# Performance work log

Hardware: AMD Instinct MI355X
Metric: run time of the kernel (lower is better)

## Reference

```python
import jax, jax.numpy as jnp
import numpy as np

LATENT, TARGET, EMB_SCALE = 2048, 64, 0.1
STEPS_IGNORE, STEPS_PREDICT = 2, 3


def conv(x, w, b, stride=(1, 1), padding=((0, 0), (0, 0))):
    y = jax.lax.conv_general_dilated(x, w, stride, padding,
                                     dimension_numbers=('NCHW', 'OIHW', 'NCHW'))
    return y + b[None, :, None, None]


def setup_inputs() -> dict:
    key = jax.random.key(0)
    ks = jax.random.split(key, 24)
    B = 64
    inp = {}
    inp['images'] = jax.random.normal(ks[0], (B, 3, 256, 256), jnp.float32)
    inp['rnd'] = jax.random.randint(ks[1], (B * 49,), 0, 16, jnp.int32)
    s = lambda *sh: 1.0 / np.sqrt(np.prod(sh[1:]))
    # stand-in encoder: conv3->256 k8 s8, relu, conv256->2048 1x1, relu, global mean pool
    inp['enc_w1'] = jax.random.normal(ks[2], (256, 3, 8, 8), jnp.float32) * s(256, 3, 8, 8)
    inp['enc_b1'] = jnp.zeros((256,), jnp.float32)
    inp['enc_w2'] = jax.random.normal(ks[3], (LATENT, 256, 1, 1), jnp.float32) * s(LATENT, 256)
    inp['enc_b2'] = jnp.zeros((LATENT,), jnp.float32)
    # PixelCNN: 5 residual blocks, each 4 convs
    inp['pc_w1'] = jax.random.normal(ks[4], (5, 256, LATENT, 1, 1), jnp.float32) * s(0, LATENT)
    inp['pc_b1'] = jnp.zeros((5, 256), jnp.float32)
    inp['pc_w2'] = jax.random.normal(ks[5], (5, 256, 256, 1, 3), jnp.float32) * s(0, 256 * 3)
    inp['pc_b2'] = jnp.zeros((5, 256), jnp.float32)
    inp['pc_w3'] = jax.random.normal(ks[6], (5, 256, 256, 2, 1), jnp.float32) * s(0, 256 * 2)
    inp['pc_b3'] = jnp.zeros((5, 256), jnp.float32)
    inp['pc_w4'] = jax.random.normal(ks[7], (5, LATENT, 256, 1, 1), jnp.float32) * s(0, 256)
    inp['pc_b4'] = jnp.zeros((5, LATENT), jnp.float32)
    inp['z2t_w'] = jax.random.normal(ks[8], (TARGET, LATENT, 1, 1), jnp.float32) * s(0, LATENT)
    inp['z2t_b'] = jnp.zeros((TARGET,), jnp.float32)
    inp['c2p_w'] = jax.random.normal(ks[9], (STEPS_PREDICT, TARGET, LATENT, 1, 1), jnp.float32) * s(0, LATENT)
    inp['c2p_b'] = jnp.zeros((STEPS_PREDICT, TARGET), jnp.float32)
    return inp


def _forward(images, enc_w1, enc_b1, enc_w2, enc_b2,
             pc_w1, pc_b1, pc_w2, pc_b2, pc_w3, pc_b3, pc_w4, pc_b4,
             z2t_w, z2t_b, c2p_w, c2p_b, rnd):
    B = images.shape[0]
    # ---- patch extraction: (B,3,256,256) -> (B*49,3,64,64), r-major then c ----
    patches = jnp.stack([images[:, :, r * 32:r * 32 + 64, c * 32:c * 32 + 64]
                         for r in range(7) for c in range(7)], axis=1)
    patches = patches.reshape(-1, 3, 64, 64)
    N = patches.shape[0]
    # ---- vectorized random border masking (replaces per-patch python loop) ----
    r = (rnd // 4).astype(jnp.int32)           # (N,)
    c = (rnd % 4).astype(jnp.int32)
    idx = jnp.arange(64, dtype=jnp.int32)
    row_ok = (idx[None, :] >= r[:, None]) & (idx[None, :] < r[:, None] + 60)  # (N,64)
    col_ok = (idx[None, :] >= c[:, None]) & (idx[None, :] < c[:, None] + 60)
    mask = row_ok[:, None, :, None] & col_ok[:, None, None, :]                # (N,1,64,64)
    patches = jnp.where(mask, patches, jnp.float32(-1.0))
    # ---- stand-in encoder (resnet_v1 replaced by small conv stack) ----
    h = jax.nn.relu(conv(patches, enc_w1, enc_b1, stride=(8, 8)))  # (N,256,8,8)
    h = jax.nn.relu(conv(h, enc_w2, enc_b2))                        # (N,2048,8,8)
    latents = h.mean(axis=(2, 3))                                   # (N,2048)
    latents = latents.reshape(B, 7, 7, LATENT).transpose(0, 3, 1, 2)  # (B,2048,7,7)
    # ---- PixelCNN context ----
    x = latents
    for k in range(5):
        y = jax.nn.relu(conv(x, pc_w1[k], pc_b1[k]))
        y = jax.nn.relu(conv(y, pc_w2[k], pc_b2[k], padding=((0, 0), (1, 1))))
        y = jax.nn.relu(conv(y, pc_w3[k], pc_b3[k], padding=((1, 0), (0, 0))))
        y = conv(y, pc_w4[k], pc_b4[k])
        x = jax.nn.relu(y + x)
    context = x
    # ---- contrastive loss ----
    targets = conv(latents, z2t_w, z2t_b).transpose(0, 2, 3, 1).reshape(-1, TARGET)  # (B*49,64)
    col_dim, row_dim = 7, 7
    loss = jnp.float32(0.0)
    for i in range(STEPS_IGNORE, STEPS_IGNORE + STEPS_PREDICT):
        col_dim_i = col_dim - i - 1
        total = B * col_dim_i * row_dim
        preds = conv(context, c2p_w[i - STEPS_IGNORE], c2p_b[i - STEPS_IGNORE])
        preds = preds[:, :, :-(i + 1), :] * EMB_SCALE
        preds = preds.transpose(0, 2, 3, 1).reshape(-1, TARGET)  # (total,64)
        logits = preds @ targets.T                                # (total, B*49)
        ar = jnp.arange(total)
        b_idx = ar // (col_dim_i * row_dim)
        col = ar % (col_dim_i * row_dim)
        labels = b_idx * (col_dim * row_dim) + (i + 1) * row_dim + col
        lsm = jax.nn.log_softmax(logits, axis=-1)
        loss = loss + (-lsm[ar, labels]).mean()
    return loss, latents.mean(axis=(2, 3))


def reference(images, rnd, enc_w1, enc_b1, enc_w2, enc_b2,
              pc_w1, pc_b1, pc_w2, pc_b2, pc_w3, pc_b3, pc_w4, pc_b4,
              z2t_w, z2t_b, c2p_w, c2p_b):
    return _forward(images, enc_w1, enc_b1, enc_w2, enc_b2,
                    pc_w1, pc_b1, pc_w2, pc_b2, pc_w3, pc_b3, pc_w4, pc_b4,
                    z2t_w, z2t_b, c2p_w, c2p_b, rnd)
```

## Files before the change

### kernel.cpp

```cpp
#include <hip/hip_runtime.h>
#include <hip/hip_bf16.h>
#include <cstdint>
#include <cstddef>

typedef __attribute__((ext_vector_type(8))) short short8;
typedef __attribute__((ext_vector_type(4))) short short4v;
typedef __attribute__((ext_vector_type(4))) float f32x4;

__device__ __forceinline__ float bf2f(unsigned short u) {
  union { unsigned int i; float f; } v; v.i = ((unsigned int)u) << 16; return v.f;
}
__device__ __forceinline__ unsigned short f2bf(float f) {
  union { float f; unsigned int i; } v; v.f = f;
  unsigned int x = v.i;
  return (unsigned short)((x + 0x7fffu + ((x >> 16) & 1u)) >> 16);
}
__device__ __forceinline__ f32x4 mfma16(short8 a, short8 b, f32x4 c) {
  return __builtin_amdgcn_mfma_f32_16x16x32_bf16(a, b, c, 0, 0, 0);
}
__device__ __forceinline__ void gload16(const void* src, void* dst) {
  __builtin_amdgcn_global_load_lds(
      (const __attribute__((address_space(1))) unsigned int*)src,
      (__attribute__((address_space(3))) unsigned int*)dst, 16, 0, 0);
}

__device__ __forceinline__ void cvt4(const float* __restrict__ src,
                                     unsigned short* __restrict__ dst, int i) {
  float4 v = reinterpret_cast<const float4*>(src)[i];
  short4v o;
  o[0] = (short)f2bf(v.x); o[1] = (short)f2bf(v.y);
  o[2] = (short)f2bf(v.z); o[3] = (short)f2bf(v.w);
  reinterpret_cast<short4v*>(dst)[i] = o;
}

__global__ __launch_bounds__(256) void k_prep(
    const float* __restrict__ enc_w1, const float* __restrict__ enc_w2,
    const float* __restrict__ pc_w1, const float* __restrict__ pc_w4,
    const float* __restrict__ z2t_w, const float* __restrict__ c2p_w,
    const float* __restrict__ pc_w2, const float* __restrict__ pc_w3,
    unsigned short* __restrict__ w1b, unsigned short* __restrict__ w2b,
    unsigned short* __restrict__ pcw1b, unsigned short* __restrict__ pcw4b,
    unsigned short* __restrict__ z2tb, unsigned short* __restrict__ c2pb,
    unsigned short* __restrict__ w2t, unsigned short* __restrict__ w3t)
{
  const int b = blockIdx.x, tid = threadIdx.x;
  if (b < 48)        cvt4(enc_w1, w1b,   b * 256 + tid);
  else if (b < 560)  cvt4(enc_w2, w2b,   (b - 48) * 256 + tid);
  else if (b < 3120) cvt4(pc_w1,  pcw1b, (b - 560) * 256 + tid);
  else if (b < 5680) cvt4(pc_w4,  pcw4b, (b - 3120) * 256 + tid);
  else if (b < 5808) cvt4(z2t_w,  z2tb,  (b - 5680) * 256 + tid);
  else if (b < 6192) cvt4(c2p_w,  c2pb,  (b - 5808) * 256 + tid);
  else if (b < 10032) {
    const int e = (b - 6192) * 256 + tid;
    const int k5 = e / 196608, r = e % 196608;
    const int co = r / 768, kk = r % 768, d = kk >> 8, ci = kk & 255;
    w2t[e] = f2bf(pc_w2[((size_t)(k5 * 256 + co) * 256 + ci) * 3 + d]);
  } else {
    const int e = (b - 10032) * 256 + tid;
    const int k5 = e / 131072, r = e % 131072;
    const int co = r >> 9, kk = r & 511, s = kk >> 8, ci = kk & 255;
    w3t[e] = f2bf(pc_w3[((size_t)(k5 * 256 + co) * 256 + ci) * 2 + s]);
  }
}

__global__ __launch_bounds__(256) void k_enc2(
    const unsigned short* __restrict__ H1, const unsigned short* __restrict__ w2b,
    const float* __restrict__ b2, unsigned short* __restrict__ xout, int gbase)
{
  __shared__ char lds[32768];
  char* At = lds;
  char* Bt = lds + 16384;
  const int tid = threadIdx.x;
  const int nwg = gridDim.x;
  int bid = blockIdx.x;
  int l = bid;
  if ((nwg & 7) == 0) { const int cpx = nwg >> 3; l = (bid & 7) * cpx + (bid >> 3); }
  const int m0 = (l & 15) * 128;
  const int by = l >> 4;
  const int w = tid >> 6, lane = tid & 63, lr = lane & 15, lg = lane >> 4;
  const int wm = w & 1, wn = w >> 1;
  const int srow = lane >> 3, sslot = lane & 7;
  f32x4 acc[4][4];
  for (int i = 0; i < 4; i++) for (int j = 0; j < 4; j++) acc[i][j] = (f32x4)0.f;
  for (int kb = 0; kb < 4; kb++) {
    __syncthreads();
#pragma unroll
    for (int c = 0; c < 4; c++) {
      const int rbase = w * 32 + c * 8;
      const int row = rbase + srow;
      gload16(w2b + (size_t)(m0 + row) * 256 + kb * 64 + ((sslot ^ (row & 7)) * 8),
              At + rbase * 128);
    }
#pragma unroll
    for (int c = 0; c < 4; c++) {
      const int rbase = w * 32 + c * 8;
      const int row = rbase + srow;
      gload16(H1 + (size_t)(by * 128 + row) * 256 + kb * 64 + ((sslot ^ (row & 7)) * 8),
              Bt + rbase * 128);
    }
    __syncthreads();
#pragma unroll
    for (int kk = 0; kk < 2; kk++) {
      const int gg = kk * 4 + lg;
      short8 bb[4];
#pragma unroll
      for (int nt = 0; nt < 4; nt++) {
        const int row = wn * 64 + nt * 16 + lr;
        bb[nt] = *reinterpret_cast<const short8*>(Bt + row * 128 + ((gg ^ (row & 7)) * 16));
      }
#pragma unroll
      for (int cot = 0; cot < 4; cot++) {
        const int row = wm * 64 + cot * 16 + lr;
        const short8 a = *reinterpret_cast<const short8*>(At + row * 128 + ((gg ^ (row & 7)) * 16));
#pragma unroll
        for (int nt = 0; nt < 4; nt++)
          acc[cot][nt] = mfma16(a, bb[nt], acc[cot][nt]);
      }
    }
  }
  const int n = gbase + by * 2 + wn;
#pragma unroll
  for (int cot = 0; cot < 4; cot++) {
    const int cob = m0 + wm * 64 + cot * 16 + lg * 4;
    float4 bi = *reinterpret_cast<const float4*>(b2 + cob);
    const float bv[4] = { bi.x, bi.y, bi.z, bi.w };
    float s[4] = { 0.f, 0.f, 0.f, 0.f };
#pragma unroll
    for (int nt = 0; nt < 4; nt++)
#pragma unroll
      for (int r = 0; r < 4; r++)
        s[r] += fmaxf(acc[cot][nt][r] + bv[r], 0.f);
#pragma unroll
    for (int r = 0; r < 4; r++)
#pragma unroll
      for (int mk = 1; mk < 16; mk <<= 1)
        s[r] += __shfl_xor(s[r], mk, 64);
    if (lr == 0) {
      short4v o;
#pragma unroll
      for (int r = 0; r < 4; r++) o[r] = (short)f2bf(s[r] * (1.f / 64.f));
      *reinterpret_cast<short4v*>(xout + (size_t)n * 2048 + cob) = o;
    }
  }
}

__global__ __launch_bounds__(256) void k_out2(const unsigned short* __restrict__ x,
                                              float* __restrict__ out) {
  const int ch = blockIdx.x * 256 + threadIdx.x;
  const int b = blockIdx.y;
  float s = 0.f;
  for (int p = 0; p < 49; p++) s += bf2f(x[(size_t)(b * 49 + p) * 2048 + ch]);
  out[1 + b * 2048 + ch] = s * (1.f / 49.f);
}

template<int M_BLK, int MODE, bool BIAS, bool RELU, bool RESID, bool SCALE, bool OBF16>
__global__ __launch_bounds__(256) void k_gemm(
    const unsigned short* __restrict__ in, const unsigned short* __restrict__ W,
    const float* __restrict__ bias, float* __restrict__ outf,
    unsigned short* __restrict__ outb, const unsigned short* __restrict__ res,
    int M, int K, int bstride, int aux, float scale,
    int wzs, int bzs, int ozs,
    const float* __restrict__ img, const int* __restrict__ rndp)
{
  constexpr int MF = M_BLK / 64;
  constexpr int AG = M_BLK * 8;
  constexpr int CHA = M_BLK / 32;
  constexpr bool DBUF = (MODE == 0 || MODE == 3);
  constexpr int BUF = (M_BLK + 64) * 128;
  __shared__ char ldsb[(DBUF ? 2 : 1) * BUF];
  const int tid = threadIdx.x;
  const int z = blockIdx.z;
  W += (size_t)z * wzs;
  if (BIAS) bias += (size_t)z * bzs;
  const int m0 = blockIdx.x * M_BLK;
  const int n0 = blockIdx.y * 64;
  const int w = tid >> 6, lane = tid & 63, lr = lane & 15, lg = lane >> 4;
  const int srow = lane >> 3, sslot = lane & 7;
  int pb = 0, pR = 0, pC = 0, roff = 0, coff = 0;
  if constexpr (MODE == 4) {
    const int pn = aux + blockIdx.y;
    pb = pn / 49; const int prc = pn % 49; pR = prc / 7; pC = prc % 7;
    const int rv = rndp[pn];
    roff = rv >> 2; coff = rv & 3;
  }
  f32x4 acc[MF][4];
  for (int mf = 0; mf < MF; mf++) for (int nt = 0; nt < 4; nt++) acc[mf][nt] = (f32x4)0.f;
  const int KB = K >> 6;

  auto stageA = [&](char* At, int kb) {
#pragma unroll
    for (int c = 0; c < CHA; c++) {
      const int rbase = w * (M_BLK / 4) + c * 8;
      const int row = rbase + srow;
      gload16(W + (size_t)(m0 + row) * K + kb * 64 + ((sslot ^ (row & 7)) * 8),
              At + rbase * 128);
    }
  };
  auto compute = [&](const char* At, const char* Bt) {
#pragma unroll
    for (int kk = 0; kk < 2; kk++) {
      short8 a[MF], bb[4];
      const int gg = kk * 4 + lg;
#pragma unroll
      for (int mf = 0; mf < MF; mf++) {
        const int row = w * (M_BLK / 4) + mf * 16 + lr;
        a[mf] = *reinterpret_cast<const short8*>(At + row * 128 + ((gg ^ (row & 7)) * 16));
      }
#pragma unroll
      for (int nt = 0; nt < 4; nt++) {
        const int row = nt * 16 + lr;
        bb[nt] = *reinterpret_cast<const short8*>(Bt + row * 128 + ((gg ^ (row & 7)) * 16));
      }
#pragma unroll
      for (int mf = 0; mf < MF; mf++)
#pragma unroll
        for (int nt = 0; nt < 4; nt++)
          acc[mf][nt] = mfma16(a[mf], bb[nt], acc[mf][nt]);
    }
  };

  if constexpr (DBUF) {
    auto stageB = [&](char* Bt, int kb) {
#pragma unroll
      for (int c = 0; c < 2; c++) {
        const int rbase = w * 16 + c * 8;
        const int row = rbase + srow;
        int n = n0 + row;
        if constexpr (MODE == 3) n = (n / aux) * 49 + (n % aux);
        gload16(in + (size_t)n * bstride + kb * 64 + ((sslot ^ (row & 7)) * 8),
                Bt + rbase * 128);
      }
    };
    stageA(ldsb, 0);
    stageB(ldsb + M_BLK * 128, 0);
    __syncthreads();
    int cur = 0;
    for (int kb = 0; kb < KB; kb++) {
      if (kb + 1 < KB) {
        char* nb = ldsb + (cur ^ 1) * BUF;
        stageA(nb, kb + 1);
        stageB(nb + M_BLK * 128, kb + 1);
      }
      char* cb = ldsb + cur * BUF;
      compute(cb, cb + M_BLK * 128);
      __syncthreads();
      cur ^= 1;
    }
  } else {
    for (int kb = 0; kb < KB; kb++) {
      __syncthreads();
      stageA(ldsb, kb);
      char* Bt = ldsb + M_BLK * 128;
      for (int g = AG + tid; g < AG + 512; g += 256) {
        const int h = g - AG, row = h >> 3, slot = h & 7;
        const int n = n0 + row;
        const int k = kb * 64 + slot * 8;
        short8 v = (short8)(short)0;
        if constexpr (MODE == 1) {
          const int d = k >> 8, ci = k & 255;
          const int wp = n % 7 + d - 1;
          if ((unsigned)wp <= 6u)
            v = *reinterpret_cast<const short8*>(in + (size_t)(n + d - 1) * 256 + ci);
        } else if constexpr (MODE == 2) {
          const int s2 = k >> 8, ci = k & 255;
          const int hh = (n % 49) / 7;
          if (hh + s2 >= 1)
            v = *reinterpret_cast<const short8*>(in + (size_t)(n + (s2 - 1) * 7) * 256 + ci);
        } else {
          const int p = row;
          const int gr = kb * 8 + slot;
          const int ci = gr >> 3, ky = gr & 7;
          const int oy = p >> 3, ox = p & 7;
          const int y = oy * 8 + ky;
          const float* src = img + (((size_t)(pb * 3 + ci) * 256 + (size_t)(pR * 32 + y)) * 256
                                    + pC * 32 + ox * 8);
          float4 v0 = *reinterpret_cast<const float4*>(src);
          float4 v1 = *reinterpret_cast<const float4*>(src + 4);
          const bool rok = (y >= roff) && (y < roff + 60);
          float vals[8] = { v0.x, v0.y, v0.z, v0.w, v1.x, v1.y, v1.z, v1.w };
          const int x0 = ox * 8;
#pragma unroll
          for (int q = 0; q < 8; q++) {
            const int xx = x0 + q;
            const bool ok = rok && (xx >= coff) && (xx < coff + 60);
            v[q] = (short)f2bf(ok ? vals[q] : -1.0f);
          }
        }
        *reinterpret_cast<short8*>(Bt + row * 128 + ((slot ^ (row & 7)) * 16)) = v;
      }
      __syncthreads();
      compute(ldsb, ldsb + M_BLK * 128);
    }
  }

#pragma unroll
  for (int mf = 0; mf < MF; mf++) {
    const int mb = m0 + w * (M_BLK / 4) + mf * 16 + lg * 4;
    float bv[4] = {0.f, 0.f, 0.f, 0.f};
    if constexpr (BIAS) {
      float4 t4 = *reinterpret_cast<const float4*>(bias + mb);
      bv[0] = t4.x; bv[1] = t4.y; bv[2] = t4.z; bv[3] = t4.w;
    }
#pragma unroll
    for (int nt = 0; nt < 4; nt++) {
      const size_t nn = (size_t)(n0 + nt * 16 + lr);
      const size_t off = nn * (size_t)M + mb + (size_t)z * ozs;
      float v[4];
#pragma unroll
      for (int r = 0; r < 4; r++) {
        v[r] = acc[mf][nt][r] + bv[r];
        if (SCALE) v[r] *= scale;
      }
      if (RESID) {
        short4v rv = *reinterpret_cast<const short4v*>(res + off);
#pragma unroll
        for (int r = 0; r < 4; r++) v[r] += bf2f((unsigned short)rv[r]);
      }
#pragma unroll
      for (int r = 0; r < 4; r++) if (RELU) v[r] = fmaxf(v[r], 0.f);
      if (OBF16) {
        short4v o;
#pragma unroll
        for (int r = 0; r < 4; r++) o[r] = (short)f2bf(v[r]);
        *reinterpret_cast<short4v*>(outb + off) = o;
      } else {
        float4 o; o.x = v[0]; o.y = v[1]; o.z = v[2]; o.w = v[3];
        *reinterpret_cast<float4*>(outf + off) = o;
      }
    }
  }
}

__global__ __launch_bounds__(256) void k_lse(const float* __restrict__ logits,
                                             float* __restrict__ lossr,
                                             int cd7, int base, int lab7)
{
  __shared__ float redM[256], redS[256];
  const int r = blockIdx.x, tid = threadIdx.x;
  const float4* row = reinterpret_cast<const float4*>(logits + (size_t)r * 3136);
  float m = -1e30f, s = 0.f;
  for (int i = tid; i < 784; i += 256) {
    float4 v4 = row[i];
    float vv[4] = { v4.x, v4.y, v4.z, v4.w };
#pragma unroll
    for (int q = 0; q < 4; q++) {
      const float nm = fmaxf(m, vv[q]);
      s = s * __expf(m - nm) + __expf(vv[q] - nm);
      m = nm;
    }
  }
  redM[tid] = m; redS[tid] = s;
  for (int off = 128; off > 0; off >>= 1) {
    __syncthreads();
    if (tid < off) {
      const float m2 = redM[tid + off], s2 = redS[tid + off];
      const float nm = fmaxf(redM[tid], m2);
      redS[tid] = redS[tid] * __expf(redM[tid] - nm) + s2 * __expf(m2 - nm);
      redM[tid] = nm;
    }
  }
  __syncthreads();
  if (tid == 0) {
    const int b = r / cd7, hw = r % cd7;
    const int lab = b * 49 + hw + lab7;
    lossr[base + r] = (redM[0] + __logf(redS[0])) - logits[(size_t)r * 3136 + lab];
  }
}

__global__ __launch_bounds__(256) void k_loss_final(const float* __restrict__ lossr,
                                                    float* __restrict__ out) {
  __shared__ float red[256];
  const int tid = threadIdx.x;
  float s = 0.f;
  for (int i = tid; i < 4032; i += 256) {
    const float wgt = (i < 1792) ? (1.f / 1792.f) : ((i < 3136) ? (1.f / 1344.f) : (1.f / 896.f));
    s += lossr[i] * wgt;
  }
  red[tid] = s;
  for (int off = 128; off > 0; off >>= 1) {
    __syncthreads();
    if (tid < off) red[tid] += red[tid + off];
  }
  if (tid == 0) out[0] = red[0];
}

extern "C" void kernel_launch(void* const* d_in, const int* in_sizes, int n_in,
                              void* d_out, int out_size, void* d_ws, size_t ws_size,
                              hipStream_t stream)
{
  (void)in_sizes; (void)n_in; (void)out_size;
  const float* images = (const float*)d_in[0];
  const int*   rnd    = (const int*)d_in[1];
  const float* enc_w1 = (const float*)d_in[2];
  const float* enc_b1 = (const float*)d_in[3];
  const float* enc_w2 = (const float*)d_in[4];
  const float* enc_b2 = (const float*)d_in[5];
  const float* pc_w1  = (const float*)d_in[6];
  const float* pc_b1  = (const float*)d_in[7];
  const float* pc_w2  = (const float*)d_in[8];
  const float* pc_b2  = (const float*)d_in[9];
  const float* pc_w3  = (const float*)d_in[10];
  const float* pc_b3  = (const float*)d_in[11];
  const float* pc_w4  = (const float*)d_in[12];
  const float* pc_b4  = (const float*)d_in[13];
  const float* z2t_w  = (const float*)d_in[14];
  const float* z2t_b  = (const float*)d_in[15];
  const float* c2p_w  = (const float*)d_in[16];
  const float* c2p_b  = (const float*)d_in[17];
  float* out = (float*)d_out;
  char* ws = (char*)d_ws;

  unsigned short* w1b    = (unsigned short*)(ws + 0);
  unsigned short* w2b    = (unsigned short*)(ws + 98304);
  unsigned short* z2tb   = (unsigned short*)(ws + 1146880);
  unsigned short* c2pb   = (unsigned short*)(ws + 1409024);
  unsigned short* w2t    = (unsigned short*)(ws + 2195456);
  unsigned short* w3t    = (unsigned short*)(ws + 4161536);
  unsigned short* targ   = (unsigned short*)(ws + 5472256);
  unsigned short* predsb = (unsigned short*)(ws + 5873664);
  float*          lossr  = (float*)(ws + 7077888);
  unsigned short* y1b    = (unsigned short*)(ws + 7094016);
  unsigned short* y2b    = (unsigned short*)(ws + 8699648);
  unsigned short* pcw1b  = (unsigned short*)(ws + 10305280);
  unsigned short* pcw4b  = (unsigned short*)(ws + 15548160);
  unsigned short* xbuf   = (unsigned short*)(ws + 20791040);
  float*          logits = (float*)(ws + 10305280);

  k_prep<<<12592, 256, 0, stream>>>(enc_w1, enc_w2, pc_w1, pc_w4, z2t_w, c2p_w,
                                    pc_w2, pc_w3,
                                    w1b, w2b, pcw1b, pcw4b, z2tb, c2pb, w2t, w3t);

  const size_t h1_off = 33636352;
  const size_t per_patch = 64 * 256 * 2;
  unsigned short* H1;
  int CH;
  if (ws_size > h1_off + 2 * per_patch) {
    size_t avail = (ws_size - h1_off) / per_patch;
    CH = (int)(avail > 3136 ? 3136 : avail) & ~1;
    H1 = (unsigned short*)(ws + h1_off);
  } else {
    H1 = y1b;
    CH = 98;
  }
  for (int base = 0; base < 3136; base += CH) {
    const int c = (3136 - base) < CH ? (3136 - base) : CH;
    k_gemm<256, 4, true, true, false, false, true><<<dim3(1, c), 256, 0, stream>>>(
        nullptr, w1b, enc_b1, nullptr, H1, nullptr, 256, 192, 0, base, 1.f,
        0, 0, 0, images, rnd);
    k_enc2<<<16 * (c / 2), 256, 0, stream>>>(H1, w2b, enc_b2, xbuf, base);
  }

  k_out2<<<dim3(8, 64), 256, 0, stream>>>(xbuf, out);
  k_gemm<64, 0, true, false, false, false, true><<<dim3(1, 49), 256, 0, stream>>>(
      xbuf, z2tb, z2t_b, nullptr, targ, nullptr, 64, 2048, 2048, 0, 1.f, 0, 0, 0,
      nullptr, nullptr);

  for (int k = 0; k < 5; k++) {
    k_gemm<64, 0, true, true, false, false, true><<<dim3(4, 49), 256, 0, stream>>>(
        xbuf, pcw1b + (size_t)k * 524288, pc_b1 + k * 256, nullptr, y1b, nullptr,
        256, 2048, 2048, 0, 1.f, 0, 0, 0, nullptr, nullptr);
    k_gemm<64, 1, true, true, false, false, true><<<dim3(4, 49), 256, 0, stream>>>(
        y1b, w2t + (size_t)k * 196608, pc_b2 + k * 256, nullptr, y2b, nullptr,
        256, 768, 256, 0, 1.f, 0, 0, 0, nullptr, nullptr);
    k_gemm<64, 2, true, true, false, false, true><<<dim3(4, 49), 256, 0, stream>>>(
        y2b, w3t + (size_t)k * 131072, pc_b3 + k * 256, nullptr, y1b, nullptr,
        256, 512, 256, 0, 1.f, 0, 0, 0, nullptr, nullptr);
    k_gemm<128, 0, true, true, true, false, true><<<dim3(16, 49), 256, 0, stream>>>(
        y1b, pcw4b + (size_t)k * 524288, pc_b4 + k * 2048, nullptr, xbuf, xbuf,
        2048, 256, 256, 0, 1.f, 0, 0, 0, nullptr, nullptr);
  }

  k_gemm<64, 0, true, false, false, true, true><<<dim3(1, 49, 3), 256, 0, stream>>>(
      xbuf, c2pb, c2p_b, nullptr, predsb, nullptr, 64, 2048, 2048, 0, 0.1f,
      131072, 64, 200704, nullptr, nullptr);

  const int cd7a[3] = {28, 21, 14};
  const int basea[3] = {0, 1792, 3136};
  for (int ip = 0; ip < 3; ip++) {
    const int rows = cd7a[ip] * 64;
    k_gemm<64, 3, false, false, false, false, false><<<dim3(49, rows / 64), 256, 0, stream>>>(
        predsb + (size_t)ip * 200704, targ, nullptr, logits, nullptr, nullptr,
        3136, 64, 64, cd7a[ip], 1.f, 0, 0, 0, nullptr, nullptr);
    k_lse<<<rows, 256, 0, stream>>>(logits, lossr, cd7a[ip], basea[ip], 7 * (ip + 3));
  }
  k_loss_final<<<1, 256, 0, stream>>>(lossr, out);
}
```

Measured before the change: 698.2 us.

## Fuse logits GEMM with online log-softmax loss; enlarge enc2 tile to 512 threads

```diff
diff --git a/kernel.cpp b/kernel.cpp
--- a/kernel.cpp
+++ b/kernel.cpp
@@ -63,83 +63,86 @@
   }
 }
 
-__global__ __launch_bounds__(256) void k_enc2(
+__global__ __launch_bounds__(512) void k_enc2(
     const unsigned short* __restrict__ H1, const unsigned short* __restrict__ w2b,
     const float* __restrict__ b2, unsigned short* __restrict__ xout, int gbase)
 {
-  __shared__ char lds[32768];
+  __shared__ char lds[49152];
   char* At = lds;
   char* Bt = lds + 16384;
   const int tid = threadIdx.x;
   const int nwg = gridDim.x;
-  int bid = blockIdx.x;
-  int l = bid;
-  if ((nwg & 7) == 0) { const int cpx = nwg >> 3; l = (bid & 7) * cpx + (bid >> 3); }
+  const int bid = blockIdx.x;
+  const int cpx = nwg >> 3;
+  const int l = (bid & 7) * cpx + (bid >> 3);
   const int m0 = (l & 15) * 128;
   const int by = l >> 4;
   const int w = tid >> 6, lane = tid & 63, lr = lane & 15, lg = lane >> 4;
-  const int wm = w & 1, wn = w >> 1;
+  const int wm = w & 3, wn = w >> 2;
   const int srow = lane >> 3, sslot = lane & 7;
-  f32x4 acc[4][4];
-  for (int i = 0; i < 4; i++) for (int j = 0; j < 4; j++) acc[i][j] = (f32x4)0.f;
+  f32x4 acc[2][8];
+  for (int i = 0; i < 2; i++) for (int j = 0; j < 8; j++) acc[i][j] = (f32x4)0.f;
   for (int kb = 0; kb < 4; kb++) {
     __syncthreads();
+#pragma unroll
+    for (int c = 0; c < 2; c++) {
+      const int rbase = w * 16 + c * 8;
+      const int row = rbase + srow;
+      gload16(w2b + (size_t)(m0 + row) * 256 + kb * 64 + ((sslot ^ (row & 7)) * 8),
+              At + rbase * 128);
+    }
 #pragma unroll
     for (int c = 0; c < 4; c++) {
       const int rbase = w * 32 + c * 8;
       const int row = rbase + srow;
-      gload16(w2b + (size_t)(m0 + row) * 256 + kb * 64 + ((sslot ^ (row & 7)) * 8),
-              At + rbase * 128);
-    }
-#pragma unroll
-    for (int c = 0; c < 4; c++) {
-      const int rbase = w * 32 + c * 8;
-      const int row = rbase + srow;
-      gload16(H1 + (size_t)(by * 128 + row) * 256 + kb * 64 + ((sslot ^ (row & 7)) * 8),
+      gload16(H1 + (size_t)(by * 256 + row) * 256 + kb * 64 + ((sslot ^ (row & 7)) * 8),
               Bt + rbase * 128);
     }
     __syncthreads();
 #pragma unroll
     for (int kk = 0; kk < 2; kk++) {
       const int gg = kk * 4 + lg;
-      short8 bb[4];
-#pragma unroll
-      for (int nt = 0; nt < 4; nt++) {
-        const int row = wn * 64 + nt * 16 + lr;
+      short8 bb[8];
+#pragma unroll
+      for (int nt = 0; nt < 8; nt++) {
+        const int row = wn * 128 + nt * 16 + lr;
         bb[nt] = *reinterpret_cast<const short8*>(Bt + row * 128 + ((gg ^ (row & 7)) * 16));
       }
 #pragma unroll
-      for (int cot = 0; cot < 4; cot++) {
-        const int row = wm * 64 + cot * 16 + lr;
+      for (int cot = 0; cot < 2; cot++) {
+        const int row = wm * 32 + cot * 16 + lr;
         const short8 a = *reinterpret_cast<const short8*>(At + row * 128 + ((gg ^ (row & 7)) * 16));
 #pragma unroll
-        for (int nt = 0; nt < 4; nt++)
+        for (int nt = 0; nt < 8; nt++)
           acc[cot][nt] = mfma16(a, bb[nt], acc[cot][nt]);
       }
     }
   }
-  const int n = gbase + by * 2 + wn;
-#pragma unroll
-  for (int cot = 0; cot < 4; cot++) {
-    const int cob = m0 + wm * 64 + cot * 16 + lg * 4;
+#pragma unroll
+  for (int cot = 0; cot < 2; cot++) {
+    const int cob = m0 + wm * 32 + cot * 16 + lg * 4;
     float4 bi = *reinterpret_cast<const float4*>(b2 + cob);
     const float bv[4] = { bi.x, bi.y, bi.z, bi.w };
-    float s[4] = { 0.f, 0.f, 0.f, 0.f };
-#pragma unroll
-    for (int nt = 0; nt < 4; nt++)
+#pragma unroll
+    for (int q = 0; q < 2; q++) {
+      float s[4] = { 0.f, 0.f, 0.f, 0.f };
+#pragma unroll
+      for (int j = 0; j < 4; j++)
+#pragma unroll
+        for (int r = 0; r < 4; r++)
+          s[r] += fmaxf(acc[cot][q * 4 + j][r] + bv[r], 0.f);
 #pragma unroll
       for (int r = 0; r < 4; r++)
-        s[r] += fmaxf(acc[cot][nt][r] + bv[r], 0.f);
-#pragma unroll
-    for (int r = 0; r < 4; r++)
-#pragma unroll
-      for (int mk = 1; mk < 16; mk <<= 1)
-        s[r] += __shfl_xor(s[r], mk, 64);
-    if (lr == 0) {
-      short4v o;
-#pragma unroll
-      for (int r = 0; r < 4; r++) o[r] = (short)f2bf(s[r] * (1.f / 64.f));
-      *reinterpret_cast<short4v*>(xout + (size_t)n * 2048 + cob) = o;
+#pragma unroll
+        for (int mk = 1; mk < 16; mk <<= 1)
+          s[r] += __shfl_xor(s[r], mk, 64);
+      if (lr == 0) {
+        const int n = gbase + by * 4 + wn * 2 + q;
+        short4v o;
+#pragma unroll
+        for (int r = 0; r < 4; r++) o[r] = (short)f2bf(s[r] * (1.f / 64.f));
+        *reinterpret_cast<short4v*>(xout + (size_t)n * 2048 + cob) = o;
+      }
     }
   }
 }
@@ -165,7 +168,7 @@
   constexpr int MF = M_BLK / 64;
   constexpr int AG = M_BLK * 8;
   constexpr int CHA = M_BLK / 32;
-  constexpr bool DBUF = (MODE == 0 || MODE == 3);
+  constexpr bool DBUF = (MODE == 0);
   constexpr int BUF = (M_BLK + 64) * 128;
   __shared__ char ldsb[(DBUF ? 2 : 1) * BUF];
   const int tid = threadIdx.x;
@@ -226,7 +229,6 @@
         const int rbase = w * 16 + c * 8;
         const int row = rbase + srow;
         int n = n0 + row;
-        if constexpr (MODE == 3) n = (n / aux) * 49 + (n % aux);
         gload16(in + (size_t)n * bstride + kb * 64 + ((sslot ^ (row & 7)) * 8),
                 Bt + rbase * 128);
       }
@@ -331,39 +333,106 @@
   }
 }
 
-__global__ __launch_bounds__(256) void k_lse(const float* __restrict__ logits,
-                                             float* __restrict__ lossr,
-                                             int cd7, int base, int lab7)
+__global__ __launch_bounds__(256) void k_lse2(
+    const unsigned short* __restrict__ predsb, const unsigned short* __restrict__ targ,
+    float* __restrict__ lossr)
 {
-  __shared__ float redM[256], redS[256];
-  const int r = blockIdx.x, tid = threadIdx.x;
-  const float4* row = reinterpret_cast<const float4*>(logits + (size_t)r * 3136);
-  float m = -1e30f, s = 0.f;
-  for (int i = tid; i < 784; i += 256) {
-    float4 v4 = row[i];
-    float vv[4] = { v4.x, v4.y, v4.z, v4.w };
-#pragma unroll
-    for (int q = 0; q < 4; q++) {
-      const float nm = fmaxf(m, vv[q]);
-      s = s * __expf(m - nm) + __expf(vv[q] - nm);
+  __shared__ char At[8192];
+  __shared__ char Bt[8192];
+  __shared__ float redM[4][64], redS[4][64], zl[64];
+  const int tid = threadIdx.x;
+  const int R0 = blockIdx.x * 64;
+  int ip, base, cd7;
+  if (R0 < 1792)      { ip = 0; base = 0;    cd7 = 28; }
+  else if (R0 < 3136) { ip = 1; base = 1792; cd7 = 21; }
+  else                { ip = 2; base = 3136; cd7 = 14; }
+  const int lab7 = 7 * (ip + 3);
+  const unsigned short* preds = predsb + (size_t)ip * 200704;
+  const int w = tid >> 6, lane = tid & 63, lr = lane & 15, lg = lane >> 4;
+  const int srow = lane >> 3, sslot = lane & 7;
+
+#pragma unroll
+  for (int c = 0; c < 2; c++) {
+    const int rbase = w * 16 + c * 8;
+    const int row = rbase + srow;
+    const int rr = R0 - base + row;
+    const int np = (rr / cd7) * 49 + (rr % cd7);
+    gload16(preds + (size_t)np * 64 + ((sslot ^ (row & 7)) * 8), Bt + rbase * 128);
+  }
+  if (tid < 64) zl[tid] = 0.f;
+
+  int labv[4];
+#pragma unroll
+  for (int nt = 0; nt < 4; nt++) {
+    const int nc = R0 - base + nt * 16 + lr;
+    labv[nt] = (nc / cd7) * 49 + (nc % cd7) + lab7;
+  }
+  float mrun[4] = {-1e30f, -1e30f, -1e30f, -1e30f};
+  float srun[4] = {0.f, 0.f, 0.f, 0.f};
+
+  for (int t = 0; t < 49; t++) {
+#pragma unroll
+    for (int c = 0; c < 2; c++) {
+      const int rbase = w * 16 + c * 8;
+      const int row = rbase + srow;
+      gload16(targ + (size_t)(t * 64 + row) * 64 + ((sslot ^ (row & 7)) * 8),
+              At + rbase * 128);
+    }
+    __syncthreads();
+    f32x4 av[4];
+#pragma unroll
+    for (int nt = 0; nt < 4; nt++) av[nt] = (f32x4)0.f;
+#pragma unroll
+    for (int kk = 0; kk < 2; kk++) {
+      const int gg = kk * 4 + lg;
+      const int arow = w * 16 + lr;
+      const short8 a = *reinterpret_cast<const short8*>(At + arow * 128 + ((gg ^ (arow & 7)) * 16));
+#pragma unroll
+      for (int nt = 0; nt < 4; nt++) {
+        const int brow = nt * 16 + lr;
+        const short8 b = *reinterpret_cast<const short8*>(Bt + brow * 128 + ((gg ^ (brow & 7)) * 16));
+        av[nt] = mfma16(a, b, av[nt]);
+      }
+    }
+    const int mg = t * 64 + w * 16 + lg * 4;
+#pragma unroll
+    for (int nt = 0; nt < 4; nt++) {
+      float v0 = av[nt][0], v1 = av[nt][1], v2 = av[nt][2], v3 = av[nt][3];
+      if (mg + 0 == labv[nt]) zl[nt * 16 + lr] = v0;
+      if (mg + 1 == labv[nt]) zl[nt * 16 + lr] = v1;
+      if (mg + 2 == labv[nt]) zl[nt * 16 + lr] = v2;
+      if (mg + 3 == labv[nt]) zl[nt * 16 + lr] = v3;
+      const float vm = fmaxf(fmaxf(v0, v1), fmaxf(v2, v3));
+      const float nm = fmaxf(mrun[nt], vm);
+      srun[nt] = srun[nt] * __expf(mrun[nt] - nm)
+               + __expf(v0 - nm) + __expf(v1 - nm) + __expf(v2 - nm) + __expf(v3 - nm);
+      mrun[nt] = nm;
+    }
+    __syncthreads();
+  }
+#pragma unroll
+  for (int nt = 0; nt < 4; nt++) {
+#pragma unroll
+    for (int mk = 16; mk < 64; mk <<= 1) {
+      const float om = __shfl_xor(mrun[nt], mk, 64);
+      const float os = __shfl_xor(srun[nt], mk, 64);
+      const float nm = fmaxf(mrun[nt], om);
+      srun[nt] = srun[nt] * __expf(mrun[nt] - nm) + os * __expf(om - nm);
+      mrun[nt] = nm;
+    }
+    if (lg == 0) { redM[w][nt * 16 + lr] = mrun[nt]; redS[w][nt * 16 + lr] = srun[nt]; }
+  }
+  __syncthreads();
+  if (tid < 64) {
+    float m = redM[0][tid], s = redS[0][tid];
+#pragma unroll
+    for (int wv = 1; wv < 4; wv++) {
+      const float om = redM[wv][tid], os = redS[wv][tid];
+      const float nm = fmaxf(m, om);
+      s = s * __expf(m - nm) + os * __expf(om - nm);
       m = nm;
     }
-  }
-  redM[tid] = m; redS[tid] = s;
-  for (int off = 128; off > 0; off >>= 1) {
-    __syncthreads();
-    if (tid < off) {
-      const float m2 = redM[tid + off], s2 = redS[tid + off];
-      const float nm = fmaxf(redM[tid], m2);
-      redS[tid] = redS[tid] * __expf(redM[tid] - nm) + s2 * __expf(m2 - nm);
-      redM[tid] = nm;
-    }
-  }
-  __syncthreads();
-  if (tid == 0) {
-    const int b = r / cd7, hw = r % cd7;
-    const int lab = b * 49 + hw + lab7;
-    lossr[base + r] = (redM[0] + __logf(redS[0])) - logits[(size_t)r * 3136 + lab];
+    lossr[R0 + tid] = (m + __logf(s)) - zl[tid];
   }
 }
 
@@ -424,7 +493,6 @@
   unsigned short* pcw1b  = (unsigned short*)(ws + 10305280);
   unsigned short* pcw4b  = (unsigned short*)(ws + 15548160);
   unsigned short* xbuf   = (unsigned short*)(ws + 20791040);
-  float*          logits = (float*)(ws + 10305280);
 
   k_prep<<<12592, 256, 0, stream>>>(enc_w1, enc_w2, pc_w1, pc_w4, z2t_w, c2p_w,
                                     pc_w2, pc_w3,
@@ -434,20 +502,20 @@
   const size_t per_patch = 64 * 256 * 2;
   unsigned short* H1;
   int CH;
-  if (ws_size > h1_off + 2 * per_patch) {
+  if (ws_size > h1_off + 4 * per_patch) {
     size_t avail = (ws_size - h1_off) / per_patch;
-    CH = (int)(avail > 3136 ? 3136 : avail) & ~1;
+    CH = (int)(avail > 3136 ? 3136 : avail) & ~3;
     H1 = (unsigned short*)(ws + h1_off);
   } else {
     H1 = y1b;
-    CH = 98;
+    CH = 96;
   }
   for (int base = 0; base < 3136; base += CH) {
     const int c = (3136 - base) < CH ? (3136 - base) : CH;
     k_gemm<256, 4, true, true, false, false, true><<<dim3(1, c), 256, 0, stream>>>(
         nullptr, w1b, enc_b1, nullptr, H1, nullptr, 256, 192, 0, base, 1.f,
         0, 0, 0, images, rnd);
-    k_enc2<<<16 * (c / 2), 256, 0, stream>>>(H1, w2b, enc_b2, xbuf, base);
+    k_enc2<<<16 * (c / 4), 512, 0, stream>>>(H1, w2b, enc_b2, xbuf, base);
   }
 
   k_out2<<<dim3(8, 64), 256, 0, stream>>>(xbuf, out);
@@ -474,14 +542,6 @@
       xbuf, c2pb, c2p_b, nullptr, predsb, nullptr, 64, 2048, 2048, 0, 0.1f,
       131072, 64, 200704, nullptr, nullptr);
 
-  const int cd7a[3] = {28, 21, 14};
-  const int basea[3] = {0, 1792, 3136};
-  for (int ip = 0; ip < 3; ip++) {
-    const int rows = cd7a[ip] * 64;
-    k_gemm<64, 3, false, false, false, false, false><<<dim3(49, rows / 64), 256, 0, stream>>>(
-        predsb + (size_t)ip * 200704, targ, nullptr, logits, nullptr, nullptr,
-        3136, 64, 64, cd7a[ip], 1.f, 0, 0, 0, nullptr, nullptr);
-    k_lse<<<rows, 256, 0, stream>>>(logits, lossr, cd7a[ip], basea[ip], 7 * (ip + 3));
-  }
+  k_lse2<<<63, 256, 0, stream>>>(predsb, targ, lossr);
   k_loss_final<<<1, 256, 0, stream>>>(lossr, out);
 }
```

Result: slower. 789.3 us (+13.0%).
